# Optimization experiments

Hardware: AMD Instinct MI355X
Metric: run time of the kernel (lower is better)

Reference implementation:

```python
import jax, jax.numpy as jnp
import numpy as np

N = 100000
NEG_SLOPE = 0.2


def gat_layer(x, src, dst, W, a_src, a_dst, b):
    # x: [N, Fin]; src/dst: [Etot] (self-loops included); W: [Fin, Fout]
    h = x @ W                                  # [N, Fout]
    s_src = h @ a_src                          # [N] per-node source score
    s_dst = h @ a_dst                          # [N] per-node dest score
    e = jax.nn.leaky_relu(s_src[src] + s_dst[dst], NEG_SLOPE)  # [Etot]
    # segment softmax over destination neighborhoods (numerically stable)
    e_max = jax.ops.segment_max(e, dst, num_segments=N)
    ex = jnp.exp(e - e_max[dst])
    denom = jax.ops.segment_sum(ex, dst, num_segments=N)
    alpha = ex / denom[dst]                    # [Etot]
    out = jax.ops.segment_sum(alpha[:, None] * h[src], dst, num_segments=N) + b
    return out, alpha


def setup_inputs() -> dict:
    key = jax.random.key(0)
    ks = jax.random.split(key, 10)
    Fin, Fh, Fo = 128, 64, 32
    x = jax.random.normal(ks[0], (N, Fin), dtype=jnp.float32)
    edge_index = jax.random.randint(ks[1], (2, 3200000), 0, N, dtype=jnp.int32)
    # Glorot-ish scaled params
    W1 = jax.random.normal(ks[2], (Fin, Fh), dtype=jnp.float32) * (1.0 / np.sqrt(Fin))
    a_src1 = jax.random.normal(ks[3], (Fh,), dtype=jnp.float32) * (1.0 / np.sqrt(Fh))
    a_dst1 = jax.random.normal(ks[4], (Fh,), dtype=jnp.float32) * (1.0 / np.sqrt(Fh))
    b1 = jnp.zeros((Fh,), dtype=jnp.float32)
    W2 = jax.random.normal(ks[5], (Fh, Fo), dtype=jnp.float32) * (1.0 / np.sqrt(Fh))
    a_src2 = jax.random.normal(ks[6], (Fo,), dtype=jnp.float32) * (1.0 / np.sqrt(Fo))
    a_dst2 = jax.random.normal(ks[7], (Fo,), dtype=jnp.float32) * (1.0 / np.sqrt(Fo))
    b2 = jnp.zeros((Fo,), dtype=jnp.float32)
    return {"x": x, "edge_index": edge_index, "W1": W1, "a_src1": a_src1,
            "a_dst1": a_dst1, "b1": b1, "W2": W2, "a_src2": a_src2,
            "a_dst2": a_dst2, "b2": b2}


def reference(x, edge_index, W1, a_src1, a_dst1, b1, W2, a_src2, a_dst2, b2):
    # PyG GATConv default add_self_loops=True: append (i, i) for every node
    loops = jnp.arange(N, dtype=edge_index.dtype)
    src = jnp.concatenate([edge_index[0], loops])
    dst = jnp.concatenate([edge_index[1], loops])
    h1, alpha1 = gat_layer(x, src, dst, W1, a_src1, a_dst1, b1)
    h1 = jax.nn.elu(h1)
    h2, alpha2 = gat_layer(h1, src, dst, W2, a_src2, a_dst2, b2)
    return h2, alpha1, alpha2
```

## Files before the change

### kernel.cpp

```cpp
#include <hip/hip_runtime.h>
#include <hip/hip_fp16.h>
#include <float.h>

#define K1E 6528

__device__ __forceinline__ float wredmax(float v){
#pragma unroll
  for (int m = 32; m >= 1; m >>= 1) v = fmaxf(v, __shfl_xor(v, m, 64));
  return v;
}
__device__ __forceinline__ float wredsum(float v){
#pragma unroll
  for (int m = 32; m >= 1; m >>= 1) v += __shfl_xor(v, m, 64);
  return v;
}
__device__ __forceinline__ int wredsumi(int v){
#pragma unroll
  for (int m = 32; m >= 1; m >>= 1) v += __shfl_xor(v, m, 64);
  return v;
}
__device__ __forceinline__ unsigned pk2(float a, float b){
  __half2 t = __floats2half2_rn(a, b);
  return __builtin_bit_cast(unsigned, t);
}

__global__ __launch_bounds__(256) void k_split(
    const int* __restrict__ ei, int E0, int total, int NB, int C1,
    unsigned* __restrict__ temp, int* __restrict__ tcounts, int* __restrict__ trunstart)
{
  __shared__ int cnt[512];
  __shared__ int pref[512];
  __shared__ unsigned stage[K1E];
  const int tid = threadIdx.x, blk = blockIdx.x;
  const int lo = blk * K1E, hi = min(lo + K1E, total);

  for (int i = tid; i < 512; i += 256) cnt[i] = 0;
  __syncthreads();
  for (int i = lo + tid; i < hi; i += 256){
    int d = (i < E0) ? ei[E0 + i] : (i - E0);
    atomicAdd(&cnt[d >> 8], 1);
  }
  __syncthreads();
  for (int i = tid; i < 512; i += 256) pref[i] = cnt[i];
  __syncthreads();
  for (int off = 1; off < 512; off <<= 1){
    int a0 = (tid >= off) ? pref[tid - off] : 0;
    int a1 = pref[tid + 256 - off];
    __syncthreads();
    pref[tid] += a0;
    pref[tid + 256] += a1;
    __syncthreads();
  }
  for (int i = tid; i < NB; i += 256){
    int c = cnt[i];
    int ex = pref[i] - c;
    tcounts[(size_t)i * C1 + blk] = c;
    trunstart[(size_t)i * C1 + blk] = ex;
    cnt[i] = ex;
  }
  __syncthreads();
  for (int i = lo + tid; i < hi; i += 256){
    int s, d;
    if (i < E0){ s = ei[i]; d = ei[E0 + i]; } else { s = i - E0; d = s; }
    int p = atomicAdd(&cnt[d >> 8], 1);
    stage[p] = ((unsigned)(d & 255) << 17) | (unsigned)s;
  }
  __syncthreads();
  for (int i = tid; i < hi - lo; i += 256) temp[(size_t)lo + i] = stage[i];
}

__global__ __launch_bounds__(256) void k_rowsum(
    const int* __restrict__ tcounts, int C1, int* __restrict__ totals)
{
  const int b = blockIdx.x;
  const int* row = tcounts + (size_t)b * C1;
  int s = 0;
  for (int k = threadIdx.x; k < C1; k += 256) s += row[k];
  s = wredsumi(s);
  __shared__ int ws[4];
  if ((threadIdx.x & 63) == 0) ws[threadIdx.x >> 6] = s;
  __syncthreads();
  if (threadIdx.x == 0) totals[b] = ws[0] + ws[1] + ws[2] + ws[3];
}

__global__ __launch_bounds__(512) void k_bases2(
    const int* __restrict__ totals, int NB, int total,
    int* __restrict__ bases, int* __restrict__ offs, int N)
{
  __shared__ int sc[512];
  const int t = threadIdx.x;
  int v = (t < NB) ? totals[t] : 0;
  sc[t] = v; __syncthreads();
  for (int off = 1; off < 512; off <<= 1){
    int a = (t >= off) ? sc[t - off] : 0;
    __syncthreads();
    sc[t] += a;
    __syncthreads();
  }
  if (t < NB) bases[t] = sc[t] - v;
  if (t == 0) offs[N] = total;
}

__global__ __launch_bounds__(512) void k_bucket(
    const unsigned* __restrict__ temp, const int* __restrict__ tcounts,
    const int* __restrict__ trunstart, const int* __restrict__ bases,
    int C1, int N, int* __restrict__ ssrc, int* __restrict__ offs)
{
  __shared__ int rloc[1024], rlen[1024];
  __shared__ int cnt[256], sc[256];
  const int b = blockIdx.x, t = threadIdx.x;
  const int bb = bases[b];
  const int node0 = b << 8;
  const int nnode = min(256, N - node0);

  for (int k = t; k < C1; k += 512){
    rlen[k] = tcounts[(size_t)b * C1 + k];
    rloc[k] = k * K1E + trunstart[(size_t)b * C1 + k];
  }
  if (t < 256) cnt[t] = 0;
  __syncthreads();
  for (int r = t; r < C1; r += 512){
    const int L = rlen[r], base = rloc[r];
    for (int q = 0; q < L; ++q) atomicAdd(&cnt[temp[base + q] >> 17], 1);
  }
  __syncthreads();
  if (t < 256) sc[t] = cnt[t];
  __syncthreads();
  for (int off = 1; off < 256; off <<= 1){
    int a = (t < 256 && t >= off) ? sc[t - off] : 0;
    __syncthreads();
    if (t < 256) sc[t] += a;
    __syncthreads();
  }
  if (t < 256){
    int ex = sc[t] - cnt[t];
    if (t < nnode) offs[node0 + t] = bb + ex;
    cnt[t] = ex;
  }
  __syncthreads();
  for (int r = t; r < C1; r += 512){
    const int L = rlen[r], base = rloc[r];
    for (int q = 0; q < L; ++q){
      unsigned v = temp[base + q];
      int p = atomicAdd(&cnt[v >> 17], 1);
      ssrc[bb + p] = (int)(v & 0x1FFFFu);
    }
  }
}

template<int FIN, int FOUT>
__global__ __launch_bounds__(256) void k_linear(
    const float* __restrict__ x, const float* __restrict__ W,
    const float* __restrict__ a_s, const float* __restrict__ a_d,
    __half* __restrict__ h16, float* __restrict__ s_src, float* __restrict__ s_dst, int n)
{
  constexpr int CK = 32;
  constexpr int NCH = FIN / CK;
  __shared__ float xs[CK][257];
  const int tid = threadIdx.x;
  const int node0 = blockIdx.x * 256;
  const int node = node0 + tid;
  const int nrow = min(256, n - node0);

  float acc[FOUT];
#pragma unroll
  for (int o = 0; o < FOUT; ++o) acc[o] = 0.f;

  for (int kc = 0; kc < NCH; ++kc){
    __syncthreads();
    const int r0 = tid >> 3;
    const int c4 = tid & 7;
#pragma unroll
    for (int p = 0; p < 8; ++p){
      int row = p * 32 + r0;
      if (row < nrow){
        const float4 v = *reinterpret_cast<const float4*>(
            x + (size_t)(node0 + row) * FIN + kc * CK + c4 * 4);
        xs[c4 * 4 + 0][row] = v.x;
        xs[c4 * 4 + 1][row] = v.y;
        xs[c4 * 4 + 2][row] = v.z;
        xs[c4 * 4 + 3][row] = v.w;
      }
    }
    __syncthreads();
#pragma unroll 8
    for (int k = 0; k < CK; ++k){
      float xv = xs[k][tid];
      const int kg = kc * CK + k;
#pragma unroll
      for (int o4 = 0; o4 < FOUT / 4; ++o4){
        const float4 w = *reinterpret_cast<const float4*>(W + (size_t)kg * FOUT + o4 * 4);
        acc[o4 * 4 + 0] = fmaf(xv, w.x, acc[o4 * 4 + 0]);
        acc[o4 * 4 + 1] = fmaf(xv, w.y, acc[o4 * 4 + 1]);
        acc[o4 * 4 + 2] = fmaf(xv, w.z, acc[o4 * 4 + 2]);
        acc[o4 * 4 + 3] = fmaf(xv, w.w, acc[o4 * 4 + 3]);
      }
    }
  }

  if (node < n){
    float vs = 0.f, vd = 0.f;
#pragma unroll
    for (int o4 = 0; o4 < FOUT / 4; ++o4){
      const float4 as = *reinterpret_cast<const float4*>(a_s + o4 * 4);
      const float4 ad = *reinterpret_cast<const float4*>(a_d + o4 * 4);
      vs += acc[o4*4+0]*as.x + acc[o4*4+1]*as.y + acc[o4*4+2]*as.z + acc[o4*4+3]*as.w;
      vd += acc[o4*4+0]*ad.x + acc[o4*4+1]*ad.y + acc[o4*4+2]*ad.z + acc[o4*4+3]*ad.w;
    }
#pragma unroll
    for (int c = 0; c < FOUT / 8; ++c){
      uint4 u;
      u.x = pk2(acc[c*8+0], acc[c*8+1]);
      u.y = pk2(acc[c*8+2], acc[c*8+3]);
      u.z = pk2(acc[c*8+4], acc[c*8+5]);
      u.w = pk2(acc[c*8+6], acc[c*8+7]);
      *reinterpret_cast<uint4*>(h16 + (size_t)node * FOUT + c * 8) = u;
    }
    s_src[node] = vs;
    s_dst[node] = vd;
  }
}

template<int F, bool ELU>
__global__ __launch_bounds__(256) void k_segment(
    const int* __restrict__ offs, const int* __restrict__ ssrc,
    const float* __restrict__ s_src, const float* __restrict__ s_dst,
    const __half* __restrict__ h16, const float* __restrict__ bias,
    float* __restrict__ out, float* __restrict__ gmv, float* __restrict__ invv, int n)
{
  constexpr int CAP = 128;
  __shared__ float ew[4][CAP];
  const int wv = threadIdx.x >> 6;
  const int lane = threadIdx.x & 63;
  const int wid = (blockIdx.x * blockDim.x + threadIdx.x) >> 6;
  const bool act = wid < n;
  int beg = 0, end = 0;
  float sd = 0.f;
  if (act){ beg = offs[wid]; end = offs[wid + 1]; sd = s_dst[wid]; }
  const int deg = end - beg;
  const bool fit = deg <= CAP;

  float m = -FLT_MAX, ssum = 0.f;
  for (int j = beg + lane; j < end; j += 64){
    int s = ssrc[j];
    float e = s_src[s] + sd;
    e = (e > 0.f) ? e : 0.2f * e;
    if (fit) ew[wv][j - beg] = e;
    if (e > m){ ssum = ssum * __expf(m - e) + 1.f; m = e; }
    else ssum += __expf(e - m);
  }
  asm volatile("s_waitcnt lgkmcnt(0)" ::: "memory");
  float gm = wredmax(m);
  float denom = wredsum(ssum * __expf(m - gm));
  float inv = 1.f / denom;
  if (act && lane == 0){ gmv[wid] = gm; invv[wid] = inv; }

  constexpr int FG = F / 8;
  constexpr int ES = 64 / FG;
  const int es = lane / FG, fg = lane % FG;
  __half2 hc0 = __float2half2_rn(0.f), hc1 = hc0, hc2 = hc0, hc3 = hc0;
  for (int j = beg; j < end; j += ES){
    int jj = j + es;
    if (jj < end){
      int s = ssrc[jj];
      float e;
      if (fit) e = ew[wv][jj - beg];
      else { e = s_src[s] + sd; e = (e > 0.f) ? e : 0.2f * e; }
      float w = __expf(e - gm) * inv;
      __half2 w2 = __float2half2_rn(w);
      const uint4 hv = *reinterpret_cast<const uint4*>(h16 + (size_t)s * F + fg * 8);
      hc0 = __hfma2(w2, __builtin_bit_cast(__half2, hv.x), hc0);
      hc1 = __hfma2(w2, __builtin_bit_cast(__half2, hv.y), hc1);
      hc2 = __hfma2(w2, __builtin_bit_cast(__half2, hv.z), hc2);
      hc3 = __hfma2(w2, __builtin_bit_cast(__half2, hv.w), hc3);
    }
  }
  float2 p0 = __half22float2(hc0), p1 = __half22float2(hc1),
         p2 = __half22float2(hc2), p3 = __half22float2(hc3);
  float a0 = p0.x, a1 = p0.y, a2 = p1.x, a3 = p1.y,
        a4 = p2.x, a5 = p2.y, a6 = p3.x, a7 = p3.y;
#pragma unroll
  for (int mm = FG; mm < 64; mm <<= 1){
    a0 += __shfl_xor(a0, mm, 64); a1 += __shfl_xor(a1, mm, 64);
    a2 += __shfl_xor(a2, mm, 64); a3 += __shfl_xor(a3, mm, 64);
    a4 += __shfl_xor(a4, mm, 64); a5 += __shfl_xor(a5, mm, 64);
    a6 += __shfl_xor(a6, mm, 64); a7 += __shfl_xor(a7, mm, 64);
  }
  if (act && lane < FG){
    float o[8] = {a0,a1,a2,a3,a4,a5,a6,a7};
#pragma unroll
    for (int q = 0; q < 8; ++q){
      float v = o[q] + bias[fg * 8 + q];
      if (ELU) v = (v > 0.f) ? v : (__expf(v) - 1.f);
      o[q] = v;
    }
    float4 w0 = {o[0],o[1],o[2],o[3]}, w1 = {o[4],o[5],o[6],o[7]};
    *reinterpret_cast<float4*>(out + (size_t)wid * F + fg * 8)     = w0;
    *reinterpret_cast<float4*>(out + (size_t)wid * F + fg * 8 + 4) = w1;
  }
}

__global__ __launch_bounds__(256) void k_pack(
    const float* __restrict__ ss1, const float* __restrict__ sd1,
    const float* __restrict__ gm1, const float* __restrict__ inv1,
    const float* __restrict__ ss2, const float* __restrict__ sd2,
    const float* __restrict__ gm2, const float* __restrict__ inv2,
    float2* __restrict__ ssp, float4* __restrict__ pkd, int N)
{
  int i = blockIdx.x * blockDim.x + threadIdx.x;
  if (i >= N) return;
  ssp[i] = make_float2(ss1[i], ss2[i]);
  pkd[2 * i]     = make_float4(sd1[i], gm1[i], inv1[i], sd2[i]);
  pkd[2 * i + 1] = make_float4(gm2[i], inv2[i], 0.f, 0.f);
}

__global__ __launch_bounds__(256) void k_alpha(
    const int* __restrict__ ei, int E0, int total, int G,
    const float2* __restrict__ ssp, const float4* __restrict__ pkd,
    float* __restrict__ a1, float* __restrict__ a2)
{
  const int t = blockIdx.x * blockDim.x + threadIdx.x;
  int sv[4], dv[4];
  bool ok[4];
#pragma unroll
  for (int q = 0; q < 4; ++q){
    int i = t + q * G;
    ok[q] = i < total;
    if (ok[q]){
      if (i < E0){ sv[q] = ei[i]; dv[q] = ei[E0 + i]; }
      else { sv[q] = i - E0; dv[q] = sv[q]; }
    }
  }
  float2 ssv[4]; float4 da[4], db[4];
#pragma unroll
  for (int q = 0; q < 4; ++q){
    if (ok[q]){
      ssv[q] = ssp[sv[q]];
      da[q]  = pkd[2 * dv[q]];
      db[q]  = pkd[2 * dv[q] + 1];
    }
  }
#pragma unroll
  for (int q = 0; q < 4; ++q){
    if (ok[q]){
      int i = t + q * G;
      float e1 = ssv[q].x + da[q].x;
      e1 = (e1 > 0.f) ? e1 : 0.2f * e1;
      a1[i] = __expf(e1 - da[q].y) * da[q].z;
      float e2 = ssv[q].y + da[q].w;
      e2 = (e2 > 0.f) ? e2 : 0.2f * e2;
      a2[i] = __expf(e2 - db[q].x) * db[q].y;
    }
  }
}

extern "C" void kernel_launch(void* const* d_in, const int* in_sizes, int n_in,
                              void* d_out, int out_size, void* d_ws, size_t ws_size,
                              hipStream_t stream)
{
  const float* x    = (const float*)d_in[0];
  const int*   ei   = (const int*)  d_in[1];
  const float* W1   = (const float*)d_in[2];
  const float* a_s1 = (const float*)d_in[3];
  const float* a_d1 = (const float*)d_in[4];
  const float* b1   = (const float*)d_in[5];
  const float* W2   = (const float*)d_in[6];
  const float* a_s2 = (const float*)d_in[7];
  const float* a_d2 = (const float*)d_in[8];
  const float* b2   = (const float*)d_in[9];

  const int N    = in_sizes[0] / 128;
  const int E0   = in_sizes[1] / 2;
  const int Etot = E0 + N;
  const int NB   = (N + 255) >> 8;
  const int C1   = (Etot + K1E - 1) / K1E;

  float* out_h2 = (float*)d_out;
  float* out_a1 = out_h2 + (size_t)N * 32;
  float* out_a2 = out_a1 + Etot;

  char* wsp = (char*)d_ws; size_t woff = 0;
  auto alloc = [&](size_t bytes)->void*{
    void* p = wsp + woff; woff += (bytes + 255) & ~(size_t)255; return p;
  };
  unsigned* temp     = (unsigned*)alloc((size_t)C1 * K1E * 4);
  int*      tcounts  = (int*)  alloc((size_t)NB * C1 * 4);
  int*      trunstart= (int*)  alloc((size_t)NB * C1 * 4);
  int*      totals   = (int*)  alloc((size_t)(NB + 1) * 4);
  int*      bases    = (int*)  alloc((size_t)(NB + 1) * 4);
  int*      offs     = (int*)  alloc(((size_t)N + 1) * 4);
  int*      ssrc     = (int*)  alloc((size_t)Etot * 4);
  __half*   h1       = (__half*)alloc((size_t)N * 64 * 2);
  float*    g1       = (float*)alloc((size_t)N * 64 * 4);
  __half*   h2l      = (__half*)alloc((size_t)N * 32 * 2);
  float*    s1s      = (float*)alloc((size_t)N * 4);
  float*    s1d      = (float*)alloc((size_t)N * 4);
  float*    s2s      = (float*)alloc((size_t)N * 4);
  float*    s2d      = (float*)alloc((size_t)N * 4);
  float*    gm1      = (float*)alloc((size_t)N * 4);
  float*    inv1     = (float*)alloc((size_t)N * 4);
  float*    gm2      = (float*)alloc((size_t)N * 4);
  float*    inv2     = (float*)alloc((size_t)N * 4);
  float2*   ssp      = (float2*)alloc((size_t)N * 8);
  float4*   pkd      = (float4*)alloc((size_t)N * 32);

  const int tb = 256;
  k_split<<<C1, 256, 0, stream>>>(ei, E0, Etot, NB, C1, temp, tcounts, trunstart);
  k_rowsum<<<NB, 256, 0, stream>>>(tcounts, C1, totals);
  k_bases2<<<1, 512, 0, stream>>>(totals, NB, Etot, bases, offs, N);
  k_bucket<<<NB, 512, 0, stream>>>(temp, tcounts, trunstart, bases, C1, N, ssrc, offs);

  const int nlb = (N + 255) / 256;
  k_linear<128, 64><<<nlb, 256, 0, stream>>>(x, W1, a_s1, a_d1, h1, s1s, s1d, N);
  k_segment<64, true><<<(N + 3) / 4, 256, 0, stream>>>(offs, ssrc, s1s, s1d, h1, b1, g1, gm1, inv1, N);
  k_linear<64, 32><<<nlb, 256, 0, stream>>>(g1, W2, a_s2, a_d2, h2l, s2s, s2d, N);
  k_segment<32, false><<<(N + 3) / 4, 256, 0, stream>>>(offs, ssrc, s2s, s2d, h2l, b2, out_h2, gm2, inv2, N);

  k_pack<<<nlb, 256, 0, stream>>>(s1s, s1d, gm1, inv1, s2s, s2d, gm2, inv2, ssp, pkd, N);
  const int G = (Etot + 3) / 4;
  k_alpha<<<(G + tb - 1) / tb, tb, 0, stream>>>(ei, E0, Etot, G, ssp, pkd, out_a1, out_a2);
}
```

Before: 360.5 us.

## Split aggregation into feature-chunked passes over chunk-major fp16 features

Feature matrices are now stored chunk-major in 16-feature slabs so that each aggregation pass gathers from a 3.2 MB slab that fits in cache instead of the full row-major table. Attention weights are computed once per layer by a new score kernel and stored as fp16 per edge, then reused by several per-chunk aggregation launches. The layer-1 output is written in fp16 and read as fp16 by the second linear. The trade-off is that ssrc and the weights are re-read once per chunk and more kernels are launched, and the extra fp16 rounding of weights and hidden features costs accuracy.

```diff
diff --git a/kernel.cpp b/kernel.cpp
--- a/kernel.cpp
+++ b/kernel.cpp
@@ -22,6 +22,9 @@
 __device__ __forceinline__ unsigned pk2(float a, float b){
   __half2 t = __floats2half2_rn(a, b);
   return __builtin_bit_cast(unsigned, t);
+}
+__device__ __forceinline__ float2 upk2(unsigned u){
+  return __half22float2(__builtin_bit_cast(__half2, u));
 }
 
 __global__ __launch_bounds__(256) void k_split(
@@ -148,13 +151,14 @@
   }
 }
 
-template<int FIN, int FOUT>
+template<int FIN, int FOUT, typename TIN>
 __global__ __launch_bounds__(256) void k_linear(
-    const float* __restrict__ x, const float* __restrict__ W,
+    const TIN* __restrict__ x, const float* __restrict__ W,
     const float* __restrict__ a_s, const float* __restrict__ a_d,
-    __half* __restrict__ h16, float* __restrict__ s_src, float* __restrict__ s_dst, int n)
-{
-  constexpr int CK = 32;
+    __half* __restrict__ hc, float* __restrict__ s_src, float* __restrict__ s_dst, int n)
+{
+  constexpr bool IN16 = sizeof(TIN) == 2;
+  constexpr int CK = IN16 ? 16 : 32;
   constexpr int NCH = FIN / CK;
   __shared__ float xs[CK][257];
   const int tid = threadIdx.x;
@@ -168,18 +172,36 @@
 
   for (int kc = 0; kc < NCH; ++kc){
     __syncthreads();
-    const int r0 = tid >> 3;
-    const int c4 = tid & 7;
-#pragma unroll
-    for (int p = 0; p < 8; ++p){
-      int row = p * 32 + r0;
-      if (row < nrow){
-        const float4 v = *reinterpret_cast<const float4*>(
-            x + (size_t)(node0 + row) * FIN + kc * CK + c4 * 4);
-        xs[c4 * 4 + 0][row] = v.x;
-        xs[c4 * 4 + 1][row] = v.y;
-        xs[c4 * 4 + 2][row] = v.z;
-        xs[c4 * 4 + 3][row] = v.w;
+    if (!IN16){
+      const int r0 = tid >> 3;
+      const int c4 = tid & 7;
+#pragma unroll
+      for (int p = 0; p < 8; ++p){
+        int row = p * 32 + r0;
+        if (row < nrow){
+          const float4 v = *reinterpret_cast<const float4*>(
+              (const float*)x + (size_t)(node0 + row) * FIN + kc * CK + c4 * 4);
+          xs[c4 * 4 + 0][row] = v.x;
+          xs[c4 * 4 + 1][row] = v.y;
+          xs[c4 * 4 + 2][row] = v.z;
+          xs[c4 * 4 + 3][row] = v.w;
+        }
+      }
+    } else {
+      const int r0 = tid >> 1;
+      const int u  = tid & 1;
+#pragma unroll
+      for (int p = 0; p < 2; ++p){
+        int row = p * 128 + r0;
+        if (row < nrow){
+          const uint4 v = *reinterpret_cast<const uint4*>(
+              (const __half*)x + (size_t)kc * n * 16 + (size_t)(node0 + row) * 16 + u * 8);
+          float2 f0 = upk2(v.x), f1 = upk2(v.y), f2 = upk2(v.z), f3 = upk2(v.w);
+          xs[u * 8 + 0][row] = f0.x; xs[u * 8 + 1][row] = f0.y;
+          xs[u * 8 + 2][row] = f1.x; xs[u * 8 + 3][row] = f1.y;
+          xs[u * 8 + 4][row] = f2.x; xs[u * 8 + 5][row] = f2.y;
+          xs[u * 8 + 6][row] = f3.x; xs[u * 8 + 7][row] = f3.y;
+        }
       }
     }
     __syncthreads();
@@ -208,25 +230,25 @@
       vd += acc[o4*4+0]*ad.x + acc[o4*4+1]*ad.y + acc[o4*4+2]*ad.z + acc[o4*4+3]*ad.w;
     }
 #pragma unroll
-    for (int c = 0; c < FOUT / 8; ++c){
-      uint4 u;
-      u.x = pk2(acc[c*8+0], acc[c*8+1]);
-      u.y = pk2(acc[c*8+2], acc[c*8+3]);
-      u.z = pk2(acc[c*8+4], acc[c*8+5]);
-      u.w = pk2(acc[c*8+6], acc[c*8+7]);
-      *reinterpret_cast<uint4*>(h16 + (size_t)node * FOUT + c * 8) = u;
+    for (int c = 0; c < FOUT / 16; ++c){
+      uint4 u0, u1;
+      u0.x = pk2(acc[c*16+ 0], acc[c*16+ 1]); u0.y = pk2(acc[c*16+ 2], acc[c*16+ 3]);
+      u0.z = pk2(acc[c*16+ 4], acc[c*16+ 5]); u0.w = pk2(acc[c*16+ 6], acc[c*16+ 7]);
+      u1.x = pk2(acc[c*16+ 8], acc[c*16+ 9]); u1.y = pk2(acc[c*16+10], acc[c*16+11]);
+      u1.z = pk2(acc[c*16+12], acc[c*16+13]); u1.w = pk2(acc[c*16+14], acc[c*16+15]);
+      __half* dst = hc + ((size_t)c * n + node) * 16;
+      *reinterpret_cast<uint4*>(dst)     = u0;
+      *reinterpret_cast<uint4*>(dst + 8) = u1;
     }
     s_src[node] = vs;
     s_dst[node] = vd;
   }
 }
 
-template<int F, bool ELU>
-__global__ __launch_bounds__(256) void k_segment(
+__global__ __launch_bounds__(256) void k_score(
     const int* __restrict__ offs, const int* __restrict__ ssrc,
     const float* __restrict__ s_src, const float* __restrict__ s_dst,
-    const __half* __restrict__ h16, const float* __restrict__ bias,
-    float* __restrict__ out, float* __restrict__ gmv, float* __restrict__ invv, int n)
+    float* __restrict__ gmv, float* __restrict__ invv, __half* __restrict__ w16, int n)
 {
   constexpr int CAP = 128;
   __shared__ float ew[4][CAP];
@@ -255,38 +277,51 @@
   float inv = 1.f / denom;
   if (act && lane == 0){ gmv[wid] = gm; invv[wid] = inv; }
 
-  constexpr int FG = F / 8;
-  constexpr int ES = 64 / FG;
-  const int es = lane / FG, fg = lane % FG;
-  __half2 hc0 = __float2half2_rn(0.f), hc1 = hc0, hc2 = hc0, hc3 = hc0;
-  for (int j = beg; j < end; j += ES){
+  for (int j = beg + lane; j < end; j += 64){
+    float e;
+    if (fit) e = ew[wv][j - beg];
+    else { e = s_src[ssrc[j]] + sd; e = (e > 0.f) ? e : 0.2f * e; }
+    w16[j] = __float2half(__expf(e - gm) * inv);
+  }
+}
+
+template<typename TOUT, bool ELU>
+__global__ __launch_bounds__(256) void k_agg(
+    const int* __restrict__ offs, const int* __restrict__ ssrc,
+    const __half* __restrict__ w16, const __half* __restrict__ hc,
+    const float* __restrict__ bias, TOUT* __restrict__ out, int ostride, int n)
+{
+  const int lane = threadIdx.x & 63;
+  const int wid = (blockIdx.x * blockDim.x + threadIdx.x) >> 6;
+  if (wid >= n) return;
+  const int beg = offs[wid], end = offs[wid + 1];
+  const int es = lane >> 1, fg = lane & 1;
+
+  __half2 c0 = __float2half2_rn(0.f), c1 = c0, c2 = c0, c3 = c0;
+  for (int j = beg; j < end; j += 32){
     int jj = j + es;
     if (jj < end){
       int s = ssrc[jj];
-      float e;
-      if (fit) e = ew[wv][jj - beg];
-      else { e = s_src[s] + sd; e = (e > 0.f) ? e : 0.2f * e; }
-      float w = __expf(e - gm) * inv;
-      __half2 w2 = __float2half2_rn(w);
-      const uint4 hv = *reinterpret_cast<const uint4*>(h16 + (size_t)s * F + fg * 8);
-      hc0 = __hfma2(w2, __builtin_bit_cast(__half2, hv.x), hc0);
-      hc1 = __hfma2(w2, __builtin_bit_cast(__half2, hv.y), hc1);
-      hc2 = __hfma2(w2, __builtin_bit_cast(__half2, hv.z), hc2);
-      hc3 = __hfma2(w2, __builtin_bit_cast(__half2, hv.w), hc3);
-    }
-  }
-  float2 p0 = __half22float2(hc0), p1 = __half22float2(hc1),
-         p2 = __half22float2(hc2), p3 = __half22float2(hc3);
+      __half2 w2 = __halves2half2(w16[jj], w16[jj]);
+      const uint4 hv = *reinterpret_cast<const uint4*>(hc + (size_t)s * 16 + fg * 8);
+      c0 = __hfma2(w2, __builtin_bit_cast(__half2, hv.x), c0);
+      c1 = __hfma2(w2, __builtin_bit_cast(__half2, hv.y), c1);
+      c2 = __hfma2(w2, __builtin_bit_cast(__half2, hv.z), c2);
+      c3 = __hfma2(w2, __builtin_bit_cast(__half2, hv.w), c3);
+    }
+  }
+  float2 p0 = __half22float2(c0), p1 = __half22float2(c1),
+         p2 = __half22float2(c2), p3 = __half22float2(c3);
   float a0 = p0.x, a1 = p0.y, a2 = p1.x, a3 = p1.y,
         a4 = p2.x, a5 = p2.y, a6 = p3.x, a7 = p3.y;
 #pragma unroll
-  for (int mm = FG; mm < 64; mm <<= 1){
+  for (int mm = 2; mm < 64; mm <<= 1){
     a0 += __shfl_xor(a0, mm, 64); a1 += __shfl_xor(a1, mm, 64);
     a2 += __shfl_xor(a2, mm, 64); a3 += __shfl_xor(a3, mm, 64);
     a4 += __shfl_xor(a4, mm, 64); a5 += __shfl_xor(a5, mm, 64);
     a6 += __shfl_xor(a6, mm, 64); a7 += __shfl_xor(a7, mm, 64);
   }
-  if (act && lane < FG){
+  if (lane < 2){
     float o[8] = {a0,a1,a2,a3,a4,a5,a6,a7};
 #pragma unroll
     for (int q = 0; q < 8; ++q){
@@ -294,9 +329,17 @@
       if (ELU) v = (v > 0.f) ? v : (__expf(v) - 1.f);
       o[q] = v;
     }
-    float4 w0 = {o[0],o[1],o[2],o[3]}, w1 = {o[4],o[5],o[6],o[7]};
-    *reinterpret_cast<float4*>(out + (size_t)wid * F + fg * 8)     = w0;
-    *reinterpret_cast<float4*>(out + (size_t)wid * F + fg * 8 + 4) = w1;
+    if constexpr (sizeof(TOUT) == 2){
+      uint4 u;
+      u.x = pk2(o[0], o[1]); u.y = pk2(o[2], o[3]);
+      u.z = pk2(o[4], o[5]); u.w = pk2(o[6], o[7]);
+      *reinterpret_cast<uint4*>((__half*)out + (size_t)wid * ostride + fg * 8) = u;
+    } else {
+      float4 w0 = {o[0],o[1],o[2],o[3]}, w1 = {o[4],o[5],o[6],o[7]};
+      float* dst = (float*)out + (size_t)wid * ostride + fg * 8;
+      *reinterpret_cast<float4*>(dst)     = w0;
+      *reinterpret_cast<float4*>(dst + 4) = w1;
+    }
   }
 }
 
@@ -390,9 +433,10 @@
   int*      bases    = (int*)  alloc((size_t)(NB + 1) * 4);
   int*      offs     = (int*)  alloc(((size_t)N + 1) * 4);
   int*      ssrc     = (int*)  alloc((size_t)Etot * 4);
-  __half*   h1       = (__half*)alloc((size_t)N * 64 * 2);
-  float*    g1       = (float*)alloc((size_t)N * 64 * 4);
-  __half*   h2l      = (__half*)alloc((size_t)N * 32 * 2);
+  __half*   h1c      = (__half*)alloc((size_t)N * 64 * 2);
+  __half*   g1c      = (__half*)alloc((size_t)N * 64 * 2);
+  __half*   h2c      = (__half*)alloc((size_t)N * 32 * 2);
+  __half*   w16      = (__half*)alloc((size_t)Etot * 2);
   float*    s1s      = (float*)alloc((size_t)N * 4);
   float*    s1d      = (float*)alloc((size_t)N * 4);
   float*    s2s      = (float*)alloc((size_t)N * 4);
@@ -411,10 +455,21 @@
   k_bucket<<<NB, 512, 0, stream>>>(temp, tcounts, trunstart, bases, C1, N, ssrc, offs);
 
   const int nlb = (N + 255) / 256;
-  k_linear<128, 64><<<nlb, 256, 0, stream>>>(x, W1, a_s1, a_d1, h1, s1s, s1d, N);
-  k_segment<64, true><<<(N + 3) / 4, 256, 0, stream>>>(offs, ssrc, s1s, s1d, h1, b1, g1, gm1, inv1, N);
-  k_linear<64, 32><<<nlb, 256, 0, stream>>>(g1, W2, a_s2, a_d2, h2l, s2s, s2d, N);
-  k_segment<32, false><<<(N + 3) / 4, 256, 0, stream>>>(offs, ssrc, s2s, s2d, h2l, b2, out_h2, gm2, inv2, N);
+  const int nsb = (N + 3) / 4;
+
+  k_linear<128, 64, float><<<nlb, 256, 0, stream>>>(x, W1, a_s1, a_d1, h1c, s1s, s1d, N);
+  k_score<<<nsb, 256, 0, stream>>>(offs, ssrc, s1s, s1d, gm1, inv1, w16, N);
+  for (int c = 0; c < 4; ++c)
+    k_agg<__half, true><<<nsb, 256, 0, stream>>>(
+        offs, ssrc, w16, h1c + (size_t)c * N * 16, b1 + c * 16,
+        g1c + (size_t)c * N * 16, 16, N);
+
+  k_linear<64, 32, __half><<<nlb, 256, 0, stream>>>(g1c, W2, a_s2, a_d2, h2c, s2s, s2d, N);
+  k_score<<<nsb, 256, 0, stream>>>(offs, ssrc, s2s, s2d, gm2, inv2, w16, N);
+  for (int c = 0; c < 2; ++c)
+    k_agg<float, false><<<nsb, 256, 0, stream>>>(
+        offs, ssrc, w16, h2c + (size_t)c * N * 16, b2 + c * 16,
+        out_h2 + c * 16, 32, N);
 
   k_pack<<<nlb, 256, 0, stream>>>(s1s, s1d, gm1, inv1, s2s, s2d, gm2, inv2, ssp, pkd, N);
   const int G = (Etot + 3) / 4;
```

After: 524.5 us. +45.5%, slower.

## Split linear output columns across blocks, fold attention vectors into W, dual-accumulate aggregation

Applied to the files above, without the earlier changes.

Precomputes W·a_src and W·a_dst in a tiny kernel so each node's attention scores can be accumulated directly from x rather than from the full output row. This lets k_linear split its output features across two blocks per node tile, halving per-thread accumulators and doubling the grid to raise occupancy, at the cost of each block reloading the same x tile. The segment aggregation loop now processes two edges per iteration into separate half2 accumulators, giving more memory loads in flight per lane.

```diff
diff --git a/kernel.cpp b/kernel.cpp
--- a/kernel.cpp
+++ b/kernel.cpp
@@ -148,23 +148,50 @@
   }
 }
 
-template<int FIN, int FOUT>
+__global__ __launch_bounds__(256) void k_wa(
+    const float* __restrict__ W1, const float* __restrict__ as1, const float* __restrict__ ad1,
+    const float* __restrict__ W2, const float* __restrict__ as2, const float* __restrict__ ad2,
+    float* __restrict__ wa)
+{
+  int t = threadIdx.x;
+  if (t < 128){
+    float s = 0.f, d = 0.f;
+    for (int o = 0; o < 64; ++o){
+      float w = W1[t * 64 + o];
+      s = fmaf(w, as1[o], s); d = fmaf(w, ad1[o], d);
+    }
+    wa[t] = s; wa[128 + t] = d;
+  } else if (t < 192){
+    int k = t - 128;
+    float s = 0.f, d = 0.f;
+    for (int o = 0; o < 32; ++o){
+      float w = W2[k * 32 + o];
+      s = fmaf(w, as2[o], s); d = fmaf(w, ad2[o], d);
+    }
+    wa[256 + k] = s; wa[320 + k] = d;
+  }
+}
+
+template<int FIN, int FOUT, int S>
 __global__ __launch_bounds__(256) void k_linear(
     const float* __restrict__ x, const float* __restrict__ W,
-    const float* __restrict__ a_s, const float* __restrict__ a_d,
+    const float* __restrict__ was, const float* __restrict__ wad,
     __half* __restrict__ h16, float* __restrict__ s_src, float* __restrict__ s_dst, int n)
 {
+  constexpr int FS = FOUT / S;
   constexpr int CK = 32;
   constexpr int NCH = FIN / CK;
   __shared__ float xs[CK][257];
   const int tid = threadIdx.x;
-  const int node0 = blockIdx.x * 256;
+  const int slice = blockIdx.x % S;
+  const int node0 = (blockIdx.x / S) * 256;
   const int node = node0 + tid;
   const int nrow = min(256, n - node0);
 
-  float acc[FOUT];
-#pragma unroll
-  for (int o = 0; o < FOUT; ++o) acc[o] = 0.f;
+  float acc[FS];
+#pragma unroll
+  for (int o = 0; o < FS; ++o) acc[o] = 0.f;
+  float vs = 0.f, vd = 0.f;
 
   for (int kc = 0; kc < NCH; ++kc){
     __syncthreads();
@@ -187,9 +214,12 @@
     for (int k = 0; k < CK; ++k){
       float xv = xs[k][tid];
       const int kg = kc * CK + k;
-#pragma unroll
-      for (int o4 = 0; o4 < FOUT / 4; ++o4){
-        const float4 w = *reinterpret_cast<const float4*>(W + (size_t)kg * FOUT + o4 * 4);
+      vs = fmaf(xv, was[kg], vs);
+      vd = fmaf(xv, wad[kg], vd);
+#pragma unroll
+      for (int o4 = 0; o4 < FS / 4; ++o4){
+        const float4 w = *reinterpret_cast<const float4*>(
+            W + (size_t)kg * FOUT + slice * FS + o4 * 4);
         acc[o4 * 4 + 0] = fmaf(xv, w.x, acc[o4 * 4 + 0]);
         acc[o4 * 4 + 1] = fmaf(xv, w.y, acc[o4 * 4 + 1]);
         acc[o4 * 4 + 2] = fmaf(xv, w.z, acc[o4 * 4 + 2]);
@@ -199,25 +229,16 @@
   }
 
   if (node < n){
-    float vs = 0.f, vd = 0.f;
-#pragma unroll
-    for (int o4 = 0; o4 < FOUT / 4; ++o4){
-      const float4 as = *reinterpret_cast<const float4*>(a_s + o4 * 4);
-      const float4 ad = *reinterpret_cast<const float4*>(a_d + o4 * 4);
-      vs += acc[o4*4+0]*as.x + acc[o4*4+1]*as.y + acc[o4*4+2]*as.z + acc[o4*4+3]*as.w;
-      vd += acc[o4*4+0]*ad.x + acc[o4*4+1]*ad.y + acc[o4*4+2]*ad.z + acc[o4*4+3]*ad.w;
-    }
-#pragma unroll
-    for (int c = 0; c < FOUT / 8; ++c){
+#pragma unroll
+    for (int c = 0; c < FS / 8; ++c){
       uint4 u;
       u.x = pk2(acc[c*8+0], acc[c*8+1]);
       u.y = pk2(acc[c*8+2], acc[c*8+3]);
       u.z = pk2(acc[c*8+4], acc[c*8+5]);
       u.w = pk2(acc[c*8+6], acc[c*8+7]);
-      *reinterpret_cast<uint4*>(h16 + (size_t)node * FOUT + c * 8) = u;
-    }
-    s_src[node] = vs;
-    s_dst[node] = vd;
+      *reinterpret_cast<uint4*>(h16 + (size_t)node * FOUT + slice * FS + c * 8) = u;
+    }
+    if (slice == 0){ s_src[node] = vs; s_dst[node] = vd; }
   }
 }
 
@@ -259,12 +280,14 @@
   constexpr int ES = 64 / FG;
   const int es = lane / FG, fg = lane % FG;
   __half2 hc0 = __float2half2_rn(0.f), hc1 = hc0, hc2 = hc0, hc3 = hc0;
-  for (int j = beg; j < end; j += ES){
-    int jj = j + es;
-    if (jj < end){
-      int s = ssrc[jj];
+  __half2 hd0 = hc0, hd1 = hc0, hd2 = hc0, hd3 = hc0;
+  for (int j = beg; j < end; j += 2 * ES){
+    const int j0 = j + es;
+    const int j1 = j + ES + es;
+    if (j0 < end){
+      int s = ssrc[j0];
       float e;
-      if (fit) e = ew[wv][jj - beg];
+      if (fit) e = ew[wv][j0 - beg];
       else { e = s_src[s] + sd; e = (e > 0.f) ? e : 0.2f * e; }
       float w = __expf(e - gm) * inv;
       __half2 w2 = __float2half2_rn(w);
@@ -274,7 +297,22 @@
       hc2 = __hfma2(w2, __builtin_bit_cast(__half2, hv.z), hc2);
       hc3 = __hfma2(w2, __builtin_bit_cast(__half2, hv.w), hc3);
     }
-  }
+    if (j1 < end){
+      int s = ssrc[j1];
+      float e;
+      if (fit) e = ew[wv][j1 - beg];
+      else { e = s_src[s] + sd; e = (e > 0.f) ? e : 0.2f * e; }
+      float w = __expf(e - gm) * inv;
+      __half2 w2 = __float2half2_rn(w);
+      const uint4 hv = *reinterpret_cast<const uint4*>(h16 + (size_t)s * F + fg * 8);
+      hd0 = __hfma2(w2, __builtin_bit_cast(__half2, hv.x), hd0);
+      hd1 = __hfma2(w2, __builtin_bit_cast(__half2, hv.y), hd1);
+      hd2 = __hfma2(w2, __builtin_bit_cast(__half2, hv.z), hd2);
+      hd3 = __hfma2(w2, __builtin_bit_cast(__half2, hv.w), hd3);
+    }
+  }
+  hc0 = __hadd2(hc0, hd0); hc1 = __hadd2(hc1, hd1);
+  hc2 = __hadd2(hc2, hd2); hc3 = __hadd2(hc3, hd3);
   float2 p0 = __half22float2(hc0), p1 = __half22float2(hc1),
          p2 = __half22float2(hc2), p3 = __half22float2(hc3);
   float a0 = p0.x, a1 = p0.y, a2 = p1.x, a3 = p1.y,
@@ -299,6 +337,7 @@
     *reinterpret_cast<float4*>(out + (size_t)wid * F + fg * 8 + 4) = w1;
   }
 }
+
 
 __global__ __launch_bounds__(256) void k_pack(
     const float* __restrict__ ss1, const float* __restrict__ sd1,
@@ -393,6 +432,7 @@
   __half*   h1       = (__half*)alloc((size_t)N * 64 * 2);
   float*    g1       = (float*)alloc((size_t)N * 64 * 4);
   __half*   h2l      = (__half*)alloc((size_t)N * 32 * 2);
+  float*    wa       = (float*)alloc(384 * 4);
   float*    s1s      = (float*)alloc((size_t)N * 4);
   float*    s1d      = (float*)alloc((size_t)N * 4);
   float*    s2s      = (float*)alloc((size_t)N * 4);
@@ -410,11 +450,15 @@
   k_bases2<<<1, 512, 0, stream>>>(totals, NB, Etot, bases, offs, N);
   k_bucket<<<NB, 512, 0, stream>>>(temp, tcounts, trunstart, bases, C1, N, ssrc, offs);
 
+  k_wa<<<1, 256, 0, stream>>>(W1, a_s1, a_d1, W2, a_s2, a_d2, wa);
+
   const int nlb = (N + 255) / 256;
-  k_linear<128, 64><<<nlb, 256, 0, stream>>>(x, W1, a_s1, a_d1, h1, s1s, s1d, N);
-  k_segment<64, true><<<(N + 3) / 4, 256, 0, stream>>>(offs, ssrc, s1s, s1d, h1, b1, g1, gm1, inv1, N);
-  k_linear<64, 32><<<nlb, 256, 0, stream>>>(g1, W2, a_s2, a_d2, h2l, s2s, s2d, N);
-  k_segment<32, false><<<(N + 3) / 4, 256, 0, stream>>>(offs, ssrc, s2s, s2d, h2l, b2, out_h2, gm2, inv2, N);
+  const int nsb = (N + 3) / 4;
+
+  k_linear<128, 64, 2><<<nlb * 2, 256, 0, stream>>>(x, W1, wa, wa + 128, h1, s1s, s1d, N);
+  k_segment<64, true><<<nsb, 256, 0, stream>>>(offs, ssrc, s1s, s1d, h1, b1, g1, gm1, inv1, N);
+  k_linear<64, 32, 2><<<nlb * 2, 256, 0, stream>>>(g1, W2, wa + 256, wa + 320, h2l, s2s, s2d, N);
+  k_segment<32, false><<<nsb, 256, 0, stream>>>(offs, ssrc, s2s, s2d, h2l, b2, out_h2, gm2, inv2, N);
 
   k_pack<<<nlb, 256, 0, stream>>>(s1s, s1d, gm1, inv1, s2s, s2d, gm2, inv2, ssp, pkd, N);
   const int G = (Etot + 3) / 4;
```

Result: faster. 348.4 us (-3.4%).
